# Optimization experiments

Measured on AMD Instinct MI355X. Metric: run time of the kernel, lower is better.

The kernel has to match this reference:

```python
import jax, jax.numpy as jnp
import numpy as np

B, S, D = 2, 2048, 1024
H, KVH, HD = 16, 4, 64


def setup_inputs() -> dict:
    key = jax.random.key(0)
    ks = jax.random.split(key, 7)
    return {
        "hidden_states": jax.random.normal(ks[0], (B, S, D), jnp.float32),
        "full_mask": jax.random.normal(ks[1], (B, 1, S, S), jnp.float32),
        "tag_mask": jax.random.normal(ks[2], (B, 1, S, S), jnp.float32),
        "wq": jax.random.normal(ks[3], (H * HD, D), jnp.float32) * 0.02,
        "wk": jax.random.normal(ks[4], (KVH * HD, D), jnp.float32) * 0.02,
        "wv": jax.random.normal(ks[5], (KVH * HD, D), jnp.float32) * 0.02,
        "wo": jax.random.normal(ks[6], (D, H * HD), jnp.float32) * 0.02,
    }


def _masked_sdpa(q, k, v, mask):
    # q,k,v: [B, h, S, HD]; mask: [B, 1, S, S] additive bias
    scale = 1.0 / jnp.sqrt(jnp.asarray(HD, q.dtype))
    w = jnp.einsum("bhqd,bhkd->bhqk", q, k) * scale + mask
    w = jax.nn.softmax(w.astype(jnp.float32), axis=-1).astype(q.dtype)
    return jnp.einsum("bhqk,bhkd->bhqd", w, v)


def _repeat_kv(x, n_rep):
    # [B, KVh, S, HD] -> [B, KVh*n_rep, S, HD]
    if n_rep == 1:
        return x
    return jnp.repeat(x, n_rep, axis=1)


def reference(hidden_states, full_mask, tag_mask, wq, wk, wv, wo):
    x = hidden_states
    q = (x @ wq.T).reshape(B, S, H, HD).transpose(0, 2, 1, 3)      # bhsd
    k = (x @ wk.T).reshape(B, S, KVH, HD).transpose(0, 2, 1, 3)
    v = (x @ wv.T).reshape(B, S, KVH, HD).transpose(0, 2, 1, 3)

    n_gq, n_lq = H // 2, H - H // 2
    n_gkv, n_lkv = KVH // 2, KVH - KVH // 2
    q_g, q_l = q[:, :n_gq], q[:, n_gq:]
    k_g, k_l = k[:, :n_gkv], k[:, n_gkv:]
    v_g, v_l = v[:, :n_gkv], v[:, n_gkv:]

    k_g = _repeat_kv(k_g, n_gq // n_gkv)
    v_g = _repeat_kv(v_g, n_gq // n_gkv)
    k_l = _repeat_kv(k_l, n_lq // n_lkv)
    v_l = _repeat_kv(v_l, n_lq // n_lkv)

    out_g = _masked_sdpa(q_g, k_g, v_g, full_mask)
    out_l = _masked_sdpa(q_l, k_l, v_l, tag_mask)
    attn = jnp.concatenate([out_g, out_l], axis=1)                  # [B,H,S,HD]
    attn = attn.transpose(0, 2, 1, 3).reshape(B, S, H * HD)
    return attn @ wo.T
```

## Files before the change

kernel.cpp:

```cpp
#include <hip/hip_runtime.h>
#include <hip/hip_bf16.h>

#define B_ 2
#define S_ 2048
#define D_ 1024
#define H_ 16
#define KVH_ 4
#define HD_ 64

#define LOG2E 1.44269504089f
#define QSCALE 0.18033688011f

typedef __attribute__((ext_vector_type(4))) float f32x4;
typedef __attribute__((ext_vector_type(16))) float f32x16;
typedef __attribute__((ext_vector_type(8))) short short8;
typedef __attribute__((ext_vector_type(2))) unsigned int uint2v;

#define DEV static __device__ __forceinline__

DEV unsigned short f2bf(float f) {
  union { float f; unsigned int u; } v; v.f = f;
  unsigned int r = v.u + 0x7FFFu + ((v.u >> 16) & 1u);
  return (unsigned short)(r >> 16);
}

DEV float fexp2(float x) {
#if __has_builtin(__builtin_amdgcn_exp2f)
  return __builtin_amdgcn_exp2f(x);
#else
  float r;
  asm("v_exp_f32 %0, %1" : "=v"(r) : "v"(x));
  return r;
#endif
}

DEV unsigned int pack_bf16(float lo, float hi) {
  float2 f2; f2.x = lo; f2.y = hi;
  __hip_bfloat162 h2 = __float22bfloat162_rn(f2);
  union { __hip_bfloat162 h; unsigned int u; } cv;
  cv.h = h2;
  return cv.u;
}

DEV void permswap(unsigned int &a, unsigned int &b) {
#if __has_builtin(__builtin_amdgcn_permlane32_swap)
  uint2v r = __builtin_amdgcn_permlane32_swap(a, b, false, false);
  a = r[0]; b = r[1];
#else
  asm("v_permlane32_swap_b32 %0, %1" : "+v"(a), "+v"(b));
#endif
}

DEV float xhalf_max(float x) {
  unsigned int ua = __builtin_bit_cast(unsigned int, x), ub;
#if __has_builtin(__builtin_amdgcn_permlane32_swap)
  uint2v r = __builtin_amdgcn_permlane32_swap(ua, ua, false, false);
  ua = r[0]; ub = r[1];
#else
  asm("v_mov_b32 %1, %0\n\tv_permlane32_swap_b32 %0, %1" : "+v"(ua), "=&v"(ub));
#endif
  return fmaxf(__builtin_bit_cast(float, ua), __builtin_bit_cast(float, ub));
}

DEV float xhalf_sum(float x) {
  unsigned int ua = __builtin_bit_cast(unsigned int, x), ub;
#if __has_builtin(__builtin_amdgcn_permlane32_swap)
  uint2v r = __builtin_amdgcn_permlane32_swap(ua, ua, false, false);
  ua = r[0]; ub = r[1];
#else
  asm("v_mov_b32 %1, %0\n\tv_permlane32_swap_b32 %0, %1" : "+v"(ua), "=&v"(ub));
#endif
  return __builtin_bit_cast(float, ua) + __builtin_bit_cast(float, ub);
}

DEV void gload_lds16(const void* g, void* l) {
  __builtin_amdgcn_global_load_lds(
      (const __attribute__((address_space(1))) unsigned int*)g,
      (__attribute__((address_space(3))) unsigned int*)l, 16, 0, 0);
}

__global__ __launch_bounds__(256) void cast_kernel(const float* __restrict__ src,
                                                   unsigned short* __restrict__ dst, int n4) {
  int i = blockIdx.x * 256 + threadIdx.x;
  if (i >= n4) return;
  float4 v = ((const float4*)src)[i];
  ushort4 o;
  o.x = f2bf(v.x); o.y = f2bf(v.y); o.z = f2bf(v.z); o.w = f2bf(v.w);
  ((ushort4*)dst)[i] = o;
}

template <int MODE>
__global__ __launch_bounds__(256) void gemm_bt(
    const unsigned short* __restrict__ A, const unsigned short* __restrict__ Bw,
    float* __restrict__ C, unsigned short* __restrict__ qb,
    unsigned short* __restrict__ kb, unsigned short* __restrict__ vb,
    int M, int N, int K, int ntn) {
  __shared__ __align__(16) unsigned short As[128 * 64];
  __shared__ __align__(16) unsigned short Bs[128 * 64];
  const int tid = threadIdx.x;
  const int lane = tid & 63, wid = tid >> 6;
  const int wr = wid >> 1, wc = wid & 1;
  const int tm = blockIdx.x / ntn, tn = blockIdx.x % ntn;
  const int row0 = tm * 128, col0 = tn * 128;
  f32x4 acc[4][4] = {};
  const int sr = tid >> 3, sc = (tid & 7) * 8;
  for (int kt = 0; kt < K; kt += 64) {
    __syncthreads();
#pragma unroll
    for (int i = 0; i < 4; ++i) {
      gload_lds16(A + (size_t)(row0 + i * 32 + sr) * K + kt + sc,
                  (void*)(As + i * 2048 + tid * 8));
      gload_lds16(Bw + (size_t)(col0 + i * 32 + sr) * K + kt + sc,
                  (void*)(Bs + i * 2048 + tid * 8));
    }
    __syncthreads();
#pragma unroll
    for (int ks = 0; ks < 64; ks += 32) {
      const int fc = ks + (lane >> 4) * 8;
      short8 af[4], bf[4];
#pragma unroll
      for (int m = 0; m < 4; ++m)
        af[m] = *(const short8*)&As[(wr * 64 + m * 16 + (lane & 15)) * 64 + fc];
#pragma unroll
      for (int n = 0; n < 4; ++n)
        bf[n] = *(const short8*)&Bs[(wc * 64 + n * 16 + (lane & 15)) * 64 + fc];
#pragma unroll
      for (int m = 0; m < 4; ++m)
#pragma unroll
        for (int n = 0; n < 4; ++n)
          acc[m][n] = __builtin_amdgcn_mfma_f32_16x16x32_bf16(af[m], bf[n], acc[m][n], 0, 0, 0);
    }
  }
#pragma unroll
  for (int m = 0; m < 4; ++m)
#pragma unroll
    for (int n = 0; n < 4; ++n)
#pragma unroll
      for (int j = 0; j < 4; ++j) {
        const int grow = row0 + wr * 64 + m * 16 + (lane >> 4) * 4 + j;
        const int gcol = col0 + wc * 64 + n * 16 + (lane & 15);
        const float v = acc[m][n][j];
        if (MODE == 0) {
          C[(size_t)grow * N + gcol] = v;
        } else {
          const int b = grow >> 11, s = grow & 2047;
          if (gcol < 1024) {
            const int hh = gcol >> 6, d = gcol & 63;
            qb[(((size_t)b * H_ + hh) * S_ + s) * HD_ + d] = f2bf(v * QSCALE);
          } else if (gcol < 1280) {
            const int kk = (gcol - 1024) >> 6, d = gcol & 63;
            kb[(((size_t)b * KVH_ + kk) * S_ + s) * HD_ + d] = f2bf(v);
          } else {
            const int kk = (gcol - 1280) >> 6, d = gcol & 63;
            vb[(((size_t)b * KVH_ + kk) * HD_ + d) * S_ + s] = f2bf(v);
          }
        }
      }
}

__global__ __launch_bounds__(256) void attn_kernel(
    const unsigned short* __restrict__ qb, const unsigned short* __restrict__ kb,
    const unsigned short* __restrict__ vb, const float* __restrict__ fmask,
    const float* __restrict__ tmask, unsigned short* __restrict__ attnb) {
  __shared__ __align__(16) unsigned short Ks[2][64 * 64];
  __shared__ __align__(16) unsigned short Vs[2][64 * 64];
  const int tid = threadIdx.x;
  const int lane = tid & 63, w = tid >> 6;
  const int l31 = lane & 31, hi = lane >> 5;

  const int swz = (blockIdx.x % 8) * 64 + blockIdx.x / 8;
  const int hh = swz & 1, qt = (swz >> 1) & 63, g = (swz >> 7) & 1, b = swz >> 8;
  const int h = g * 8 + hh * 4 + w;
  const int kvh = g * 2 + hh;

  const unsigned short* kbase = kb + ((size_t)b * KVH_ + kvh) * S_ * HD_;
  const unsigned short* vbase = vb + ((size_t)b * KVH_ + kvh) * HD_ * S_;
  const float* mline = (g ? tmask : fmask) +
      ((size_t)b * S_ + qt * 32 + l31) * S_;

  short8 bq[4];
  {
    const unsigned short* qrow =
        qb + (((size_t)b * H_ + h) * S_ + qt * 32 + l31) * HD_;
#pragma unroll
    for (int ks = 0; ks < 4; ++ks)
      bq[ks] = *(const short8*)(qrow + ks * 16 + hi * 8);
  }

  f32x16 accO[2] = {};
  float mrow = -1e30f, lrow = 0.f;

  const int krow = tid >> 3, kblk = tid & 7;

#define STAGE(KT, BUF)                                                                   \
  do {                                                                                   \
    gload_lds16(kbase + (size_t)((KT) + krow) * 64 + ((kblk ^ (krow & 7)) << 3),         \
                (void*)&Ks[BUF][tid * 8]);                                               \
    gload_lds16(kbase + (size_t)((KT) + 32 + krow) * 64 + ((kblk ^ (krow & 7)) << 3),    \
                (void*)&Ks[BUF][2048 + tid * 8]);                                        \
    gload_lds16(vbase + (size_t)krow * 2048 + (KT) + ((kblk ^ (krow & 7)) << 3),         \
                (void*)&Vs[BUF][tid * 8]);                                               \
    gload_lds16(vbase + (size_t)(32 + krow) * 2048 + (KT) + ((kblk ^ (krow & 7)) << 3),  \
                (void*)&Vs[BUF][2048 + tid * 8]);                                        \
  } while (0)

#define MPREF(T, MK)                                                                     \
  do {                                                                                   \
    _Pragma("unroll")                                                                    \
    for (int u = 0; u < 2; ++u)                                                          \
      _Pragma("unroll")                                                                  \
      for (int rg = 0; rg < 4; ++rg)                                                     \
        MK[u][rg] = *(const f32x4*)&mline[(T) * 64 + u * 32 + rg * 8 + hi * 4];          \
  } while (0)

#define TILE(T, CUR, MKC, MKN)                                                           \
  do {                                                                                   \
    if ((T) + 1 < 32) MPREF((T) + 1, MKN);                                               \
    __builtin_amdgcn_sched_barrier(0);                                                   \
    if ((T) + 1 < 32) {                                                                  \
      STAGE(((T) + 1) * 64, CUR ^ 1);                                                    \
      asm volatile("s_waitcnt vmcnt(12)" ::: "memory");                                  \
    } else {                                                                             \
      asm volatile("s_waitcnt vmcnt(0)" ::: "memory");                                   \
    }                                                                                    \
    __builtin_amdgcn_s_barrier();                                                        \
    __builtin_amdgcn_sched_barrier(0);                                                   \
    const unsigned short* ksb = &Ks[CUR][0];                                             \
    const unsigned short* vsb = &Vs[CUR][0];                                             \
    _Pragma("unroll")                                                                    \
    for (int u = 0; u < 2; ++u) {                                                        \
      f32x16 s = {};                                                                     \
      __builtin_amdgcn_s_setprio(1);                                                     \
      _Pragma("unroll")                                                                  \
      for (int ks = 0; ks < 4; ++ks) {                                                   \
        short8 ak = *(const short8*)&ksb[(u * 32 + l31) * 64 +                           \
                                         (((ks * 2 + hi) ^ (lane & 7)) << 3)];           \
        s = __builtin_amdgcn_mfma_f32_32x32x16_bf16(ak, bq[ks], s, 0, 0, 0);             \
      }                                                                                  \
      __builtin_amdgcn_s_setprio(0);                                                     \
      float tmax0 = -1e30f, tmax1 = -1e30f;                                              \
      _Pragma("unroll")                                                                  \
      for (int rg = 0; rg < 4; ++rg) {                                                   \
        float v0 = fmaf(MKC[u][rg][0], LOG2E, s[rg * 4 + 0]);                            \
        float v1 = fmaf(MKC[u][rg][1], LOG2E, s[rg * 4 + 1]);                            \
        float v2 = fmaf(MKC[u][rg][2], LOG2E, s[rg * 4 + 2]);                            \
        float v3 = fmaf(MKC[u][rg][3], LOG2E, s[rg * 4 + 3]);                            \
        s[rg * 4 + 0] = v0; s[rg * 4 + 1] = v1;                                          \
        s[rg * 4 + 2] = v2; s[rg * 4 + 3] = v3;                                          \
        tmax0 = fmaxf(tmax0, fmaxf(v0, v1));                                             \
        tmax1 = fmaxf(tmax1, fmaxf(v2, v3));                                             \
      }                                                                                  \
      float tmax = xhalf_max(fmaxf(tmax0, tmax1));                                       \
      if (__any(tmax > mrow + 11.5f)) {                                                  \
        const float mnew = fmaxf(mrow, tmax);                                            \
        const float es = fexp2(mrow - mnew);                                             \
        mrow = mnew;                                                                     \
        lrow *= es;                                                                      \
        _Pragma("unroll")                                                                \
        for (int r = 0; r < 16; ++r) {                                                   \
          const float esb = __shfl(es, (r & 3) + 8 * (r >> 2) + 4 * hi);                 \
          accO[0][r] *= esb;                                                             \
          accO[1][r] *= esb;                                                             \
        }                                                                                \
      }                                                                                  \
      float rs0 = 0.f, rs1 = 0.f, rs2 = 0.f, rs3 = 0.f;                                  \
      _Pragma("unroll")                                                                  \
      for (int r = 0; r < 16; r += 4) {                                                  \
        float p0 = fexp2(s[r + 0] - mrow);                                               \
        float p1 = fexp2(s[r + 1] - mrow);                                               \
        float p2 = fexp2(s[r + 2] - mrow);                                               \
        float p3 = fexp2(s[r + 3] - mrow);                                               \
        s[r + 0] = p0; s[r + 1] = p1; s[r + 2] = p2; s[r + 3] = p3;                      \
        rs0 += p0; rs1 += p1; rs2 += p2; rs3 += p3;                                      \
      }                                                                                  \
      lrow += xhalf_sum((rs0 + rs1) + (rs2 + rs3));                                      \
      unsigned int Dw[8];                                                                \
      _Pragma("unroll")                                                                  \
      for (int i = 0; i < 8; ++i)                                                        \
        Dw[i] = pack_bf16(s[2 * i], s[2 * i + 1]);                                       \
      permswap(Dw[0], Dw[2]); permswap(Dw[1], Dw[3]);                                    \
      permswap(Dw[4], Dw[6]); permswap(Dw[5], Dw[7]);                                    \
      short8 ap[2];                                                                      \
      _Pragma("unroll")                                                                  \
      for (int k2 = 0; k2 < 2; ++k2) {                                                   \
        union { unsigned int wd[4]; short8 v; } cv;                                      \
        cv.wd[0] = Dw[k2 * 4 + 0]; cv.wd[1] = Dw[k2 * 4 + 1];                            \
        cv.wd[2] = Dw[k2 * 4 + 2]; cv.wd[3] = Dw[k2 * 4 + 3];                            \
        ap[k2] = cv.v;                                                                   \
      }                                                                                  \
      __builtin_amdgcn_s_setprio(1);                                                     \
      _Pragma("unroll")                                                                  \
      for (int dt = 0; dt < 2; ++dt)                                                     \
        _Pragma("unroll")                                                                \
        for (int k2 = 0; k2 < 2; ++k2) {                                                 \
          short8 bv = *(const short8*)&vsb[(dt * 32 + l31) * 64 +                        \
                                           (((u * 4 + k2 * 2 + hi) ^ (lane & 7)) << 3)]; \
          accO[dt] = __builtin_amdgcn_mfma_f32_32x32x16_bf16(ap[k2], bv, accO[dt], 0, 0, 0); \
        }                                                                                \
      __builtin_amdgcn_s_setprio(0);                                                     \
    }                                                                                    \
    __builtin_amdgcn_s_barrier();                                                        \
    __builtin_amdgcn_sched_barrier(0);                                                   \
  } while (0)

  f32x4 mkA[2][4], mkB[2][4];
  MPREF(0, mkA);
  STAGE(0, 0);
  for (int tt = 0; tt < 16; ++tt) {
    TILE(2 * tt, 0, mkA, mkB);
    TILE(2 * tt + 1, 1, mkB, mkA);
  }
#undef TILE
#undef MPREF
#undef STAGE

#pragma unroll
  for (int r = 0; r < 16; ++r) {
    const int crow = (r & 3) + 8 * (r >> 2) + 4 * hi;
    const float linv = 1.0f / __shfl(lrow, crow);
    const size_t o = (size_t)(b * S_ + qt * 32 + crow) * (H_ * HD_) + h * 64 + l31;
    attnb[o] = f2bf(accO[0][r] * linv);
    attnb[o + 32] = f2bf(accO[1][r] * linv);
  }
}

extern "C" void kernel_launch(void* const* d_in, const int* in_sizes, int n_in,
                              void* d_out, int out_size, void* d_ws, size_t ws_size,
                              hipStream_t stream) {
  (void)in_sizes; (void)n_in; (void)out_size; (void)ws_size;
  const float* x = (const float*)d_in[0];
  const float* fmask = (const float*)d_in[1];
  const float* tmask = (const float*)d_in[2];
  const float* wq = (const float*)d_in[3];
  const float* wk = (const float*)d_in[4];
  const float* wv = (const float*)d_in[5];
  const float* wo = (const float*)d_in[6];

  unsigned short* ws = (unsigned short*)d_ws;
  unsigned short* xb = ws;
  unsigned short* wqkvb = xb + (size_t)4096 * 1024;
  unsigned short* wob = wqkvb + (size_t)1536 * 1024;
  unsigned short* qbuf = wob + (size_t)1024 * 1024;
  unsigned short* kbuf = qbuf + (size_t)4096 * 1024;
  unsigned short* vbuf = kbuf + (size_t)1024 * 1024;
  unsigned short* attnb = vbuf + (size_t)1024 * 1024;

  cast_kernel<<<4096, 256, 0, stream>>>(x, xb, 1048576);
  cast_kernel<<<1024, 256, 0, stream>>>(wq, wqkvb, 262144);
  cast_kernel<<<256, 256, 0, stream>>>(wk, wqkvb + (size_t)1024 * 1024, 65536);
  cast_kernel<<<256, 256, 0, stream>>>(wv, wqkvb + (size_t)1280 * 1024, 65536);
  cast_kernel<<<1024, 256, 0, stream>>>(wo, wob, 262144);

  gemm_bt<1><<<32 * 12, 256, 0, stream>>>(xb, wqkvb, nullptr, qbuf, kbuf, vbuf,
                                          4096, 1536, 1024, 12);
  attn_kernel<<<512, 256, 0, stream>>>(qbuf, kbuf, vbuf, fmask, tmask, attnb);
  gemm_bt<0><<<32 * 8, 256, 0, stream>>>(attnb, wob, (float*)d_out,
                                         nullptr, nullptr, nullptr, 4096, 1024, 1024, 8);
}
```

Before: 168.0 us.

## Split attention into single-wave blocks with 32-key tiles and no barriers

The attention kernel now launches 2048 one-wave blocks instead of 512 four-wave blocks. Each wave handles one query head, stages its own K/V tiles of 32 keys (swizzled) and prefetches mask lines per tile. This drops the workgroup barriers, shrinks LDS use per block and raises the number of independent blocks. The cost is that K/V tiles are no longer shared across the four query heads of a KV group, so K/V load traffic rises and leans on L2, and each 64-key step becomes two smaller tiles with more loop overhead.

```diff
diff --git a/kernel.cpp b/kernel.cpp
--- a/kernel.cpp
+++ b/kernel.cpp
@@ -158,19 +158,19 @@
       }
 }
 
-__global__ __launch_bounds__(256) void attn_kernel(
+__global__ __launch_bounds__(64) void attn_kernel(
     const unsigned short* __restrict__ qb, const unsigned short* __restrict__ kb,
     const unsigned short* __restrict__ vb, const float* __restrict__ fmask,
     const float* __restrict__ tmask, unsigned short* __restrict__ attnb) {
-  __shared__ __align__(16) unsigned short Ks[2][64 * 64];
-  __shared__ __align__(16) unsigned short Vs[2][64 * 64];
-  const int tid = threadIdx.x;
-  const int lane = tid & 63, w = tid >> 6;
+  __shared__ __align__(16) unsigned short Ks[2][32 * 64];
+  __shared__ __align__(16) unsigned short Vs[2][32 * 64];
+  const int lane = threadIdx.x;
   const int l31 = lane & 31, hi = lane >> 5;
 
-  const int swz = (blockIdx.x % 8) * 64 + blockIdx.x / 8;
-  const int hh = swz & 1, qt = (swz >> 1) & 63, g = (swz >> 7) & 1, b = swz >> 8;
-  const int h = g * 8 + hh * 4 + w;
+  const int swz = (blockIdx.x % 8) * 256 + blockIdx.x / 8;
+  const int hw = swz & 3, qt = (swz >> 2) & 63;
+  const int hh = (swz >> 8) & 1, g = (swz >> 9) & 1, b = swz >> 10;
+  const int h = g * 8 + hh * 4 + hw;
   const int kvh = g * 2 + hh;
 
   const unsigned short* kbase = kb + ((size_t)b * KVH_ + kvh) * S_ * HD_;
@@ -190,123 +190,116 @@
   f32x16 accO[2] = {};
   float mrow = -1e30f, lrow = 0.f;
 
-  const int krow = tid >> 3, kblk = tid & 7;
+  const int krow8 = lane >> 3, kchunk = lane & 7;
+  const int sw = kchunk ^ krow8;
+  const int vd_hi = (sw >> 2) & 1;
+  const int vkv8 = (sw & 3) * 8;
 
 #define STAGE(KT, BUF)                                                                   \
   do {                                                                                   \
-    gload_lds16(kbase + (size_t)((KT) + krow) * 64 + ((kblk ^ (krow & 7)) << 3),         \
-                (void*)&Ks[BUF][tid * 8]);                                               \
-    gload_lds16(kbase + (size_t)((KT) + 32 + krow) * 64 + ((kblk ^ (krow & 7)) << 3),    \
-                (void*)&Ks[BUF][2048 + tid * 8]);                                        \
-    gload_lds16(vbase + (size_t)krow * 2048 + (KT) + ((kblk ^ (krow & 7)) << 3),         \
-                (void*)&Vs[BUF][tid * 8]);                                               \
-    gload_lds16(vbase + (size_t)(32 + krow) * 2048 + (KT) + ((kblk ^ (krow & 7)) << 3),  \
-                (void*)&Vs[BUF][2048 + tid * 8]);                                        \
+    _Pragma("unroll")                                                                    \
+    for (int i = 0; i < 4; ++i)                                                          \
+      gload_lds16(kbase + (size_t)((KT) + i * 8 + krow8) * 64 + sw * 8,                  \
+                  (void*)&Ks[BUF][i * 512 + lane * 8]);                                  \
+    _Pragma("unroll")                                                                    \
+    for (int i = 0; i < 4; ++i)                                                          \
+      gload_lds16(vbase + (size_t)(i * 8 + krow8 + vd_hi * 32) * 2048 + (KT) + vkv8,     \
+                  (void*)&Vs[BUF][i * 512 + lane * 8]);                                  \
   } while (0)
 
 #define MPREF(T, MK)                                                                     \
   do {                                                                                   \
     _Pragma("unroll")                                                                    \
-    for (int u = 0; u < 2; ++u)                                                          \
-      _Pragma("unroll")                                                                  \
-      for (int rg = 0; rg < 4; ++rg)                                                     \
-        MK[u][rg] = *(const f32x4*)&mline[(T) * 64 + u * 32 + rg * 8 + hi * 4];          \
+    for (int rg = 0; rg < 4; ++rg)                                                       \
+      MK[rg] = *(const f32x4*)&mline[(T) * 32 + rg * 8 + hi * 4];                        \
   } while (0)
 
 #define TILE(T, CUR, MKC, MKN)                                                           \
   do {                                                                                   \
-    if ((T) + 1 < 32) MPREF((T) + 1, MKN);                                               \
-    __builtin_amdgcn_sched_barrier(0);                                                   \
-    if ((T) + 1 < 32) {                                                                  \
-      STAGE(((T) + 1) * 64, CUR ^ 1);                                                    \
+    if ((T) + 1 < 64) {                                                                  \
+      MPREF((T) + 1, MKN);                                                               \
+      STAGE(((T) + 1) * 32, CUR ^ 1);                                                    \
       asm volatile("s_waitcnt vmcnt(12)" ::: "memory");                                  \
     } else {                                                                             \
       asm volatile("s_waitcnt vmcnt(0)" ::: "memory");                                   \
     }                                                                                    \
-    __builtin_amdgcn_s_barrier();                                                        \
     __builtin_amdgcn_sched_barrier(0);                                                   \
     const unsigned short* ksb = &Ks[CUR][0];                                             \
     const unsigned short* vsb = &Vs[CUR][0];                                             \
-    _Pragma("unroll")                                                                    \
-    for (int u = 0; u < 2; ++u) {                                                        \
-      f32x16 s = {};                                                                     \
-      __builtin_amdgcn_s_setprio(1);                                                     \
+    f32x16 s = {};                                                                       \
+    __builtin_amdgcn_s_setprio(1);                                                       \
+    _Pragma("unroll")                                                                    \
+    for (int ks = 0; ks < 4; ++ks) {                                                     \
+      short8 ak = *(const short8*)&ksb[l31 * 64 + (((ks * 2 + hi) ^ (l31 & 7)) << 3)];   \
+      s = __builtin_amdgcn_mfma_f32_32x32x16_bf16(ak, bq[ks], s, 0, 0, 0);               \
+    }                                                                                    \
+    __builtin_amdgcn_s_setprio(0);                                                       \
+    float tmax0 = -1e30f, tmax1 = -1e30f;                                                \
+    _Pragma("unroll")                                                                    \
+    for (int rg = 0; rg < 4; ++rg) {                                                     \
+      float v0 = fmaf(MKC[rg][0], LOG2E, s[rg * 4 + 0]);                                 \
+      float v1 = fmaf(MKC[rg][1], LOG2E, s[rg * 4 + 1]);                                 \
+      float v2 = fmaf(MKC[rg][2], LOG2E, s[rg * 4 + 2]);                                 \
+      float v3 = fmaf(MKC[rg][3], LOG2E, s[rg * 4 + 3]);                                 \
+      s[rg * 4 + 0] = v0; s[rg * 4 + 1] = v1;                                            \
+      s[rg * 4 + 2] = v2; s[rg * 4 + 3] = v3;                                            \
+      tmax0 = fmaxf(tmax0, fmaxf(v0, v1));                                               \
+      tmax1 = fmaxf(tmax1, fmaxf(v2, v3));                                               \
+    }                                                                                    \
+    float tmax = xhalf_max(fmaxf(tmax0, tmax1));                                         \
+    if (__any(tmax > mrow + 11.5f)) {                                                    \
+      const float mnew = fmaxf(mrow, tmax);                                              \
+      const float es = fexp2(mrow - mnew);                                               \
+      mrow = mnew;                                                                       \
+      lrow *= es;                                                                        \
       _Pragma("unroll")                                                                  \
-      for (int ks = 0; ks < 4; ++ks) {                                                   \
-        short8 ak = *(const short8*)&ksb[(u * 32 + l31) * 64 +                           \
-                                         (((ks * 2 + hi) ^ (lane & 7)) << 3)];           \
-        s = __builtin_amdgcn_mfma_f32_32x32x16_bf16(ak, bq[ks], s, 0, 0, 0);             \
+      for (int r = 0; r < 16; ++r) {                                                     \
+        const float esb = __shfl(es, (r & 3) + 8 * (r >> 2) + 4 * hi);                   \
+        accO[0][r] *= esb;                                                               \
+        accO[1][r] *= esb;                                                               \
       }                                                                                  \
-      __builtin_amdgcn_s_setprio(0);                                                     \
-      float tmax0 = -1e30f, tmax1 = -1e30f;                                              \
-      _Pragma("unroll")                                                                  \
-      for (int rg = 0; rg < 4; ++rg) {                                                   \
-        float v0 = fmaf(MKC[u][rg][0], LOG2E, s[rg * 4 + 0]);                            \
-        float v1 = fmaf(MKC[u][rg][1], LOG2E, s[rg * 4 + 1]);                            \
-        float v2 = fmaf(MKC[u][rg][2], LOG2E, s[rg * 4 + 2]);                            \
-        float v3 = fmaf(MKC[u][rg][3], LOG2E, s[rg * 4 + 3]);                            \
-        s[rg * 4 + 0] = v0; s[rg * 4 + 1] = v1;                                          \
-        s[rg * 4 + 2] = v2; s[rg * 4 + 3] = v3;                                          \
-        tmax0 = fmaxf(tmax0, fmaxf(v0, v1));                                             \
-        tmax1 = fmaxf(tmax1, fmaxf(v2, v3));                                             \
-      }                                                                                  \
-      float tmax = xhalf_max(fmaxf(tmax0, tmax1));                                       \
-      if (__any(tmax > mrow + 11.5f)) {                                                  \
-        const float mnew = fmaxf(mrow, tmax);                                            \
-        const float es = fexp2(mrow - mnew);                                             \
-        mrow = mnew;                                                                     \
-        lrow *= es;                                                                      \
-        _Pragma("unroll")                                                                \
-        for (int r = 0; r < 16; ++r) {                                                   \
-          const float esb = __shfl(es, (r & 3) + 8 * (r >> 2) + 4 * hi);                 \
-          accO[0][r] *= esb;                                                             \
-          accO[1][r] *= esb;                                                             \
-        }                                                                                \
-      }                                                                                  \
-      float rs0 = 0.f, rs1 = 0.f, rs2 = 0.f, rs3 = 0.f;                                  \
-      _Pragma("unroll")                                                                  \
-      for (int r = 0; r < 16; r += 4) {                                                  \
-        float p0 = fexp2(s[r + 0] - mrow);                                               \
-        float p1 = fexp2(s[r + 1] - mrow);                                               \
-        float p2 = fexp2(s[r + 2] - mrow);                                               \
-        float p3 = fexp2(s[r + 3] - mrow);                                               \
-        s[r + 0] = p0; s[r + 1] = p1; s[r + 2] = p2; s[r + 3] = p3;                      \
-        rs0 += p0; rs1 += p1; rs2 += p2; rs3 += p3;                                      \
-      }                                                                                  \
-      lrow += xhalf_sum((rs0 + rs1) + (rs2 + rs3));                                      \
-      unsigned int Dw[8];                                                                \
-      _Pragma("unroll")                                                                  \
-      for (int i = 0; i < 8; ++i)                                                        \
-        Dw[i] = pack_bf16(s[2 * i], s[2 * i + 1]);                                       \
-      permswap(Dw[0], Dw[2]); permswap(Dw[1], Dw[3]);                                    \
-      permswap(Dw[4], Dw[6]); permswap(Dw[5], Dw[7]);                                    \
-      short8 ap[2];                                                                      \
+    }                                                                                    \
+    float rs0 = 0.f, rs1 = 0.f, rs2 = 0.f, rs3 = 0.f;                                    \
+    _Pragma("unroll")                                                                    \
+    for (int r = 0; r < 16; r += 4) {                                                    \
+      float p0 = fexp2(s[r + 0] - mrow);                                                 \
+      float p1 = fexp2(s[r + 1] - mrow);                                                 \
+      float p2 = fexp2(s[r + 2] - mrow);                                                 \
+      float p3 = fexp2(s[r + 3] - mrow);                                                 \
+      s[r + 0] = p0; s[r + 1] = p1; s[r + 2] = p2; s[r + 3] = p3;                        \
+      rs0 += p0; rs1 += p1; rs2 += p2; rs3 += p3;                                        \
+    }                                                                                    \
+    lrow += xhalf_sum((rs0 + rs1) + (rs2 + rs3));                                        \
+    unsigned int Dw[8];                                                                  \
+    _Pragma("unroll")                                                                    \
+    for (int i = 0; i < 8; ++i)                                                          \
+      Dw[i] = pack_bf16(s[2 * i], s[2 * i + 1]);                                         \
+    permswap(Dw[0], Dw[2]); permswap(Dw[1], Dw[3]);                                      \
+    permswap(Dw[4], Dw[6]); permswap(Dw[5], Dw[7]);                                      \
+    short8 ap[2];                                                                        \
+    _Pragma("unroll")                                                                    \
+    for (int k2 = 0; k2 < 2; ++k2) {                                                     \
+      union { unsigned int wd[4]; short8 v; } cv;                                        \
+      cv.wd[0] = Dw[k2 * 4 + 0]; cv.wd[1] = Dw[k2 * 4 + 1];                              \
+      cv.wd[2] = Dw[k2 * 4 + 2]; cv.wd[3] = Dw[k2 * 4 + 3];                              \
+      ap[k2] = cv.v;                                                                     \
+    }                                                                                    \
+    __builtin_amdgcn_s_setprio(1);                                                       \
+    _Pragma("unroll")                                                                    \
+    for (int dt = 0; dt < 2; ++dt)                                                       \
       _Pragma("unroll")                                                                  \
       for (int k2 = 0; k2 < 2; ++k2) {                                                   \
-        union { unsigned int wd[4]; short8 v; } cv;                                      \
-        cv.wd[0] = Dw[k2 * 4 + 0]; cv.wd[1] = Dw[k2 * 4 + 1];                            \
-        cv.wd[2] = Dw[k2 * 4 + 2]; cv.wd[3] = Dw[k2 * 4 + 3];                            \
-        ap[k2] = cv.v;                                                                   \
+        short8 bv = *(const short8*)&vsb[l31 * 64 +                                      \
+                                         (((dt * 4 + k2 * 2 + hi) ^ (l31 & 7)) << 3)];   \
+        accO[dt] = __builtin_amdgcn_mfma_f32_32x32x16_bf16(ap[k2], bv, accO[dt], 0, 0, 0); \
       }                                                                                  \
-      __builtin_amdgcn_s_setprio(1);                                                     \
-      _Pragma("unroll")                                                                  \
-      for (int dt = 0; dt < 2; ++dt)                                                     \
-        _Pragma("unroll")                                                                \
-        for (int k2 = 0; k2 < 2; ++k2) {                                                 \
-          short8 bv = *(const short8*)&vsb[(dt * 32 + l31) * 64 +                        \
-                                           (((u * 4 + k2 * 2 + hi) ^ (lane & 7)) << 3)]; \
-          accO[dt] = __builtin_amdgcn_mfma_f32_32x32x16_bf16(ap[k2], bv, accO[dt], 0, 0, 0); \
-        }                                                                                \
-      __builtin_amdgcn_s_setprio(0);                                                     \
-    }                                                                                    \
-    __builtin_amdgcn_s_barrier();                                                        \
-    __builtin_amdgcn_sched_barrier(0);                                                   \
+    __builtin_amdgcn_s_setprio(0);                                                       \
   } while (0)
 
-  f32x4 mkA[2][4], mkB[2][4];
+  f32x4 mkA[4], mkB[4];
   MPREF(0, mkA);
   STAGE(0, 0);
-  for (int tt = 0; tt < 16; ++tt) {
+  for (int tt = 0; tt < 32; ++tt) {
     TILE(2 * tt, 0, mkA, mkB);
     TILE(2 * tt + 1, 1, mkB, mkA);
   }
@@ -353,7 +346,7 @@
 
   gemm_bt<1><<<32 * 12, 256, 0, stream>>>(xb, wqkvb, nullptr, qbuf, kbuf, vbuf,
                                           4096, 1536, 1024, 12);
-  attn_kernel<<<512, 256, 0, stream>>>(qbuf, kbuf, vbuf, fmask, tmask, attnb);
+  attn_kernel<<<2048, 64, 0, stream>>>(qbuf, kbuf, vbuf, fmask, tmask, attnb);
   gemm_bt<0><<<32 * 8, 256, 0, stream>>>(attnb, wob, (float*)d_out,
                                          nullptr, nullptr, nullptr, 4096, 1024, 1024, 8);
 }
```

Result: slower. 177.3 us (+5.5%).
